# Kernel optimization log

Measured on AMD Instinct MI355X. Metric: run time of the kernel, lower is better.

## Reference

```python
import jax, jax.numpy as jnp
import numpy as np

N, E = 20000, 100000
D_IN, H1, C1 = 512, 8, 64   # conv1: 512 -> 8 heads x 64, concat -> 512
H2, C2 = 4, 128             # conv2: 512 -> 4 heads x 128, mean -> 128


def setup_inputs() -> dict:
    key = jax.random.key(0)
    k = jax.random.split(key, 12)
    s_in = 1.0 / np.sqrt(D_IN).astype(np.float32)
    return {
        "street_embedding": jax.random.normal(k[0], (N, D_IN), jnp.float32),
        "edge_index": jax.random.randint(k[1], (2, E), 0, N),
        "y": jax.random.randint(k[2], (N,), 0, C2),
        "train_mask": jax.random.bernoulli(k[3], 0.5, (N,)),
        "W1": jax.random.normal(k[4], (D_IN, H1 * C1), jnp.float32) * s_in,
        "att_src1": jax.random.normal(k[5], (H1, C1), jnp.float32) * 0.1,
        "att_dst1": jax.random.normal(k[6], (H1, C1), jnp.float32) * 0.1,
        "b1": jnp.zeros((H1 * C1,), jnp.float32),
        "W2": jax.random.normal(k[7], (H1 * C1, H2 * C2), jnp.float32) * s_in,
        "att_src2": jax.random.normal(k[8], (H2, C2), jnp.float32) * 0.1,
        "att_dst2": jax.random.normal(k[9], (H2, C2), jnp.float32) * 0.1,
        "b2": jnp.zeros((C2,), jnp.float32),
    }


def _gat_conv(x, W, a_src, a_dst, b, src, dst, n, H, C, concat):
    # linear transform (no bias, as in PyG GATConv's internal lin)
    xp = (x @ W).reshape(n, H, C)                      # [N,H,C]
    asrc = jnp.einsum('nhc,hc->nh', xp, a_src)         # [N,H]
    adst = jnp.einsum('nhc,hc->nh', xp, a_dst)
    e = jax.nn.leaky_relu(asrc[src] + adst[dst], 0.2)  # [E',H] edge scores
    # softmax over incoming edges per destination node
    m = jax.lax.stop_gradient(jax.ops.segment_max(e, dst, num_segments=n))
    ex = jnp.exp(e - m[dst])
    denom = jax.ops.segment_sum(ex, dst, num_segments=n)
    alpha = ex / (denom[dst] + 1e-16)                  # [E',H]
    out = jax.ops.segment_sum(alpha[:, :, None] * xp[src], dst, num_segments=n)  # [N,H,C]
    if concat:
        return out.reshape(n, H * C) + b
    return out.mean(axis=1) + b


def reference(street_embedding, edge_index, y, train_mask,
              W1, att_src1, att_dst1, b1, W2, att_src2, att_dst2, b2):
    n = street_embedding.shape[0]
    loop = jnp.arange(n)
    # PyG GATConv adds self-loops by default
    src = jnp.concatenate([edge_index[0], loop])
    dst = jnp.concatenate([edge_index[1], loop])
    # dropout layers are identity in eval mode
    h = _gat_conv(street_embedding, W1, att_src1, att_dst1, b1, src, dst, n, H1, C1, True)
    h = jax.nn.elu(h)
    out = _gat_conv(h, W2, att_src2, att_dst2, b2, src, dst, n, H2, C2, False)  # [N,C2]
    # CrossEntropyLoss, mean over train_mask nodes (weighted mean, jit-safe)
    logp = jax.nn.log_softmax(out, axis=-1)
    ce = -jnp.take_along_axis(logp, y[:, None], axis=-1)[:, 0]
    w = train_mask.astype(out.dtype)
    loss_su = jnp.sum(w * ce) / jnp.sum(w)
    return (loss_su, out)
```

## Files before the change

kernel.cpp:

```cpp
#include <hip/hip_runtime.h>
#include <cmath>

#define D_IN 512
#define HC   512
#define NH1  8
#define NC1  64
#define NH2  4
#define NC2  128
#define BM 128
#define BN 128
#define BK 64

typedef __attribute__((ext_vector_type(8))) short short8;
typedef __attribute__((ext_vector_type(4))) float f32x4;

__device__ inline ushort f2bf(float f) {
  unsigned u = __float_as_uint(f);
  return (ushort)((u + 0x7FFFu + ((u >> 16) & 1u)) >> 16);
}
__device__ inline float bf2f(ushort b) { return __uint_as_float(((unsigned)b) << 16); }

__global__ void k_cast_all(const float* __restrict__ x, ushort* __restrict__ Abf,
                           const float* __restrict__ W1, const float* __restrict__ W2,
                           ushort* __restrict__ Wt1, ushort* __restrict__ Wt2, int n4x) {
  const int KN = D_IN * HC;
  int i = blockIdx.x * blockDim.x + threadIdx.x;
  if (i < n4x) {
    float4 v = ((const float4*)x)[i];
    ushort4 r = { f2bf(v.x), f2bf(v.y), f2bf(v.z), f2bf(v.w) };
    ((ushort4*)Abf)[i] = r;
  } else {
    int idx = i - n4x;
    if (idx >= 2 * KN) return;
    const float* W = (idx < KN) ? W1 : W2;
    ushort* Wt = (idx < KN) ? Wt1 : Wt2;
    int j = (idx < KN) ? idx : idx - KN;
    int n = j / D_IN, k = j - n * D_IN;
    Wt[j] = f2bf(W[(size_t)k * HC + n]);
  }
}

template<int H>
__global__ void k_gemm_bf16(const ushort* __restrict__ A, const ushort* __restrict__ Bt,
                            ushort* __restrict__ Cbf,
                            const float* __restrict__ att_s, const float* __restrict__ att_d,
                            float* __restrict__ asrc, float* __restrict__ adst, int M) {
  constexpr int C = HC / H;
  __shared__ __align__(16) ushort As[BM * BK];
  __shared__ __align__(16) ushort Bs[BN * BK];
  int t = threadIdx.x;
  int m0 = blockIdx.y * BM;
  int n0 = blockIdx.x * BN;
  int wave = t >> 6, lane = t & 63;
  int ln = lane & 15, qd = lane >> 4;
  int wm = (wave >> 1) * 64, wn = (wave & 1) * 64;

  f32x4 acc[4][4] = {};

  int g = t >> 6, ct = (t >> 4) & 3, lt = t & 15;
  int rA0 = m0 + g * 16 + lt;      if (rA0 > M - 1) rA0 = M - 1;
  int rA1 = m0 + 64 + g * 16 + lt; if (rA1 > M - 1) rA1 = M - 1;
  const ushort* gA0 = A + (size_t)rA0 * D_IN + ct * 8;
  const ushort* gA1 = A + (size_t)rA1 * D_IN + ct * 8;
  const ushort* gB0 = Bt + (size_t)(n0 + g * 16 + lt) * D_IN + ct * 8;
  const ushort* gB1 = Bt + (size_t)(n0 + 64 + g * 16 + lt) * D_IN + ct * 8;

  for (int k0 = 0; k0 < D_IN; k0 += BK) {
    __syncthreads();
#pragma unroll
    for (int h = 0; h < 2; ++h) {
      int ko = k0 + h * 32;
      int lo = h * 4096;
      __builtin_amdgcn_global_load_lds(
          (const __attribute__((address_space(1))) void*)(gA0 + ko),
          (__attribute__((address_space(3))) void*)(As + lo + t * 8), 16, 0, 0);
      __builtin_amdgcn_global_load_lds(
          (const __attribute__((address_space(1))) void*)(gA1 + ko),
          (__attribute__((address_space(3))) void*)(As + lo + 2048 + t * 8), 16, 0, 0);
      __builtin_amdgcn_global_load_lds(
          (const __attribute__((address_space(1))) void*)(gB0 + ko),
          (__attribute__((address_space(3))) void*)(Bs + lo + t * 8), 16, 0, 0);
      __builtin_amdgcn_global_load_lds(
          (const __attribute__((address_space(1))) void*)(gB1 + ko),
          (__attribute__((address_space(3))) void*)(Bs + lo + 2048 + t * 8), 16, 0, 0);
    }
    __syncthreads();
#pragma unroll
    for (int h = 0; h < 2; ++h) {
      int lo = h * 4096;
      short8 a[4], bb[4];
#pragma unroll
      for (int i = 0; i < 4; ++i)
        a[i] = *(const short8*)&As[lo + (((wave >> 1) * 4 + i) * 4 + qd) * 128 + ln * 8];
#pragma unroll
      for (int j = 0; j < 4; ++j)
        bb[j] = *(const short8*)&Bs[lo + (((wave & 1) * 4 + j) * 4 + qd) * 128 + ln * 8];
#pragma unroll
      for (int i = 0; i < 4; ++i)
#pragma unroll
        for (int j = 0; j < 4; ++j)
          acc[i][j] = __builtin_amdgcn_mfma_f32_16x16x32_bf16(a[i], bb[j], acc[i][j], 0, 0, 0);
    }
  }

#pragma unroll
  for (int i = 0; i < 4; ++i) {
#pragma unroll
    for (int reg = 0; reg < 4; ++reg) {
      int row = m0 + wm + i * 16 + qd * 4 + reg;
      if (row >= M) continue;
#pragma unroll
      for (int j = 0; j < 4; ++j)
        Cbf[(size_t)row * HC + n0 + wn + j * 16 + ln] = f2bf(acc[i][j][reg]);
    }
  }

  int colbase = n0 + wn;
  int h = colbase / C;
  float sa[4], da[4];
#pragma unroll
  for (int j = 0; j < 4; ++j) {
    int c = (colbase % C) + j * 16 + ln;
    sa[j] = att_s[h * C + c];
    da[j] = att_d[h * C + c];
  }
#pragma unroll
  for (int i = 0; i < 4; ++i) {
#pragma unroll
    for (int reg = 0; reg < 4; ++reg) {
      float ps = acc[i][0][reg] * sa[0] + acc[i][1][reg] * sa[1]
               + acc[i][2][reg] * sa[2] + acc[i][3][reg] * sa[3];
      float pd = acc[i][0][reg] * da[0] + acc[i][1][reg] * da[1]
               + acc[i][2][reg] * da[2] + acc[i][3][reg] * da[3];
#pragma unroll
      for (int o = 1; o < 16; o <<= 1) { ps += __shfl_xor(ps, o); pd += __shfl_xor(pd, o); }
      int row = m0 + wm + i * 16 + qd * 4 + reg;
      if (ln == 0 && row < M) {
        if (C == 64) {
          asrc[row * H + h] = ps; adst[row * H + h] = pd;
        } else {
          int sub = (colbase >> 6) & 1;
          asrc[(row * H + h) * 2 + sub] = ps;
          adst[(row * H + h) * 2 + sub] = pd;
        }
      }
    }
  }
}

__global__ void k_hist(const int* __restrict__ ei, int E, int Etot, int* __restrict__ cnt) {
  int e = blockIdx.x * blockDim.x + threadIdx.x;
  if (e >= Etot) return;
  int d = (e < E) ? ei[E + e] : e - E;
  atomicAdd(&cnt[d], 1);
}

__global__ void k_scan(const int* __restrict__ cnt, int* __restrict__ rowstart, int N) {
  int tid = threadIdx.x;
  int T = (N + 1023) / 1024;
  int base = tid * T;
  int sum = 0;
  for (int i = 0; i < T; ++i) { int j = base + i; if (j < N) sum += cnt[j]; }
  int lane = tid & 63, w = tid >> 6;
  int v = sum;
#pragma unroll
  for (int off = 1; off < 64; off <<= 1) {
    int u = __shfl_up(v, off);
    if (lane >= off) v += u;
  }
  __shared__ int wsum[16];
  if (lane == 63) wsum[w] = v;
  __syncthreads();
  if (tid < 16) {
    int tv = wsum[tid];
#pragma unroll
    for (int off = 1; off < 16; off <<= 1) {
      int u = __shfl_up(tv, off);
      if (tid >= off) tv += u;
    }
    wsum[tid] = tv;
  }
  __syncthreads();
  int wave_prefix = (w == 0) ? 0 : wsum[w - 1];
  int run = wave_prefix + v - sum;
  for (int i = 0; i < T; ++i) {
    int j = base + i;
    if (j < N) { rowstart[j] = run; run += cnt[j]; }
  }
  if (tid == 1023) rowstart[N] = run;
}

__global__ void k_scatter(const int* __restrict__ ei, int E, int Etot,
                          const int* __restrict__ rowstart, int* __restrict__ cursor,
                          int* __restrict__ csr_src) {
  int e = blockIdx.x * blockDim.x + threadIdx.x;
  if (e >= Etot) return;
  int s = (e < E) ? ei[e] : e - E;
  int d = (e < E) ? ei[E + e] : e - E;
  int pos = atomicAdd(&cursor[d], 1);
  csr_src[rowstart[d] + pos] = s;
}

template<int H, int MODE>
__global__ void k_agg(const int* __restrict__ rowstart, const int* __restrict__ csr_src,
                      const float* __restrict__ asrc, const float* __restrict__ adst,
                      const ushort* __restrict__ xp, ushort* __restrict__ hout,
                      float* __restrict__ out2, const float* __restrict__ bias,
                      const int* __restrict__ y, const int* __restrict__ msk,
                      float* __restrict__ acc2, int N) {
  int n = blockIdx.x;
  int tid = threadIdx.x;
  constexpr int C = HC / H;
  int h = (tid * 4) / C;
  int beg = rowstart[n], end = rowstart[n + 1];

  __shared__ int   s_src[32];
  __shared__ float s_out[512];

  float adn = (MODE == 1) ? adst[n * H + h]
                          : adst[(n * H + h) * 2] + adst[(n * H + h) * 2 + 1];
  float ax = 0.f, ay = 0.f, az = 0.f, aw = 0.f, wsum = 0.f;

#define SCORE(s) ((MODE == 1) ? asrc[(s) * H + h] \
                              : asrc[((s) * H + h) * 2] + asrc[((s) * H + h) * 2 + 1])

  for (int c0 = beg; c0 < end; c0 += 32) {
    int len = end - c0; if (len > 32) len = 32;
    __syncthreads();
    if (tid < len) s_src[tid] = csr_src[c0 + tid];
    __syncthreads();
    int i = 0;
    for (; i + 1 < len; i += 2) {
      int s0 = s_src[i], s1 = s_src[i + 1];
      float v0 = SCORE(s0) + adn;
      float v1 = SCORE(s1) + adn;
      ushort4 a0 = ((const ushort4*)xp)[(size_t)s0 * 128 + tid];
      ushort4 a1 = ((const ushort4*)xp)[(size_t)s1 * 128 + tid];
      v0 = (v0 > 0.f) ? v0 : 0.2f * v0;
      v1 = (v1 > 0.f) ? v1 : 0.2f * v1;
      float w0 = __expf(v0), w1 = __expf(v1);
      ax += w0 * bf2f(a0.x) + w1 * bf2f(a1.x);
      ay += w0 * bf2f(a0.y) + w1 * bf2f(a1.y);
      az += w0 * bf2f(a0.z) + w1 * bf2f(a1.z);
      aw += w0 * bf2f(a0.w) + w1 * bf2f(a1.w);
      wsum += w0 + w1;
    }
    if (i < len) {
      int s0 = s_src[i];
      float v0 = SCORE(s0) + adn;
      ushort4 a0 = ((const ushort4*)xp)[(size_t)s0 * 128 + tid];
      v0 = (v0 > 0.f) ? v0 : 0.2f * v0;
      float w0 = __expf(v0);
      ax += w0 * bf2f(a0.x); ay += w0 * bf2f(a0.y);
      az += w0 * bf2f(a0.z); aw += w0 * bf2f(a0.w);
      wsum += w0;
    }
  }
#undef SCORE
  float rdn = 1.0f / (wsum + 1e-16f);
  ax *= rdn; ay *= rdn; az *= rdn; aw *= rdn;

  if (MODE == 1) {
    int hc = tid * 4;
    float v0 = ax + bias[hc], v1 = ay + bias[hc + 1];
    float v2 = az + bias[hc + 2], v3 = aw + bias[hc + 3];
    v0 = (v0 > 0.f) ? v0 : expm1f(v0);
    v1 = (v1 > 0.f) ? v1 : expm1f(v1);
    v2 = (v2 > 0.f) ? v2 : expm1f(v2);
    v3 = (v3 > 0.f) ? v3 : expm1f(v3);
    ushort4 rr = { f2bf(v0), f2bf(v1), f2bf(v2), f2bf(v3) };
    ((ushort4*)hout)[(size_t)n * 128 + tid] = rr;
  } else {
    int hc = tid * 4;
    s_out[hc] = ax; s_out[hc + 1] = ay; s_out[hc + 2] = az; s_out[hc + 3] = aw;
    __syncthreads();
    if (tid < 32) {
#pragma unroll
      for (int k = 0; k < 4; ++k) {
        int c = tid * 4 + k;
        float sum = s_out[c] + s_out[128 + c] + s_out[256 + c] + s_out[384 + c];
        float lg = sum * 0.25f + bias[c];
        out2[(size_t)n * NC2 + c] = lg;
        s_out[c] = lg;
      }
    }
    __syncthreads();
    float lv = s_out[tid];
    int lane = tid & 63, wv = tid >> 6;
    float mx = lv;
#pragma unroll
    for (int o = 32; o > 0; o >>= 1) mx = fmaxf(mx, __shfl_xor(mx, o));
    if (lane == 0) s_out[256 + wv] = mx;
    __syncthreads();
    mx = fmaxf(s_out[256], s_out[257]);
    float e = __expf(lv - mx);
#pragma unroll
    for (int o = 32; o > 0; o >>= 1) e += __shfl_xor(e, o);
    if (lane == 0) s_out[260 + wv] = e;
    __syncthreads();
    if (tid == 0 && msk[n] != 0) {
      float se = s_out[260] + s_out[261];
      float ce = mx + logf(se) - s_out[y[n]];
      int slot = n & 127;
      atomicAdd(&acc2[slot], ce);
      atomicAdd(&acc2[128 + slot], 1.0f);
    }
  }
}

__global__ void k_final(const float* __restrict__ acc2, float* __restrict__ out0) {
  int tid = threadIdx.x;
  float ce = acc2[tid], ct = acc2[128 + tid];
#pragma unroll
  for (int o = 32; o > 0; o >>= 1) { ce += __shfl_xor(ce, o); ct += __shfl_xor(ct, o); }
  __shared__ float s[4];
  if ((tid & 63) == 0) { s[(tid >> 6) * 2] = ce; s[(tid >> 6) * 2 + 1] = ct; }
  __syncthreads();
  if (tid == 0) out0[0] = (s[0] + s[2]) / (s[1] + s[3]);
}

extern "C" void kernel_launch(void* const* d_in, const int* in_sizes, int n_in,
                              void* d_out, int out_size, void* d_ws, size_t ws_size,
                              hipStream_t stream) {
  const float* x   = (const float*)d_in[0];
  const int*   ei  = (const int*)d_in[1];
  const int*   y   = (const int*)d_in[2];
  const int*   msk = (const int*)d_in[3];
  const float* W1  = (const float*)d_in[4];
  const float* as1 = (const float*)d_in[5];
  const float* ad1 = (const float*)d_in[6];
  const float* b1  = (const float*)d_in[7];
  const float* W2  = (const float*)d_in[8];
  const float* as2 = (const float*)d_in[9];
  const float* ad2 = (const float*)d_in[10];
  const float* b2  = (const float*)d_in[11];
  float* out = (float*)d_out;

  int N = in_sizes[0] / D_IN;
  int E = in_sizes[1] / 2;
  int Etot = E + N;

  float* ws = (float*)d_ws;
  size_t NF = (size_t)N * HC;
  float* asr1 = ws;
  float* adt1 = asr1 + (size_t)N * NH1;
  float* asr2 = adt1 + (size_t)N * NH1;
  float* adt2 = asr2 + (size_t)N * 2 * NH2;
  float* acc2 = adt2 + (size_t)N * 2 * NH2;
  int*   cnt    = (int*)(acc2 + 256);
  int*   cursor = cnt + N;
  size_t zero_bytes = (256 + 2 * (size_t)N) * sizeof(float);
  int*   rowstart = cursor + N;
  int*   csr_src  = rowstart + N + 1;
  ushort* xpbf = (ushort*)((((uintptr_t)(csr_src + Etot)) + 15) & ~(uintptr_t)15);
  ushort* Abf = xpbf + NF;
  ushort* Wt1 = Abf + NF;
  ushort* Wt2 = Wt1 + (size_t)D_IN * HC;

  hipMemsetAsync(acc2, 0, zero_bytes, stream);

  int n4x = (int)(NF / 4);
  int cast_total = n4x + 2 * D_IN * HC;
  k_cast_all<<<(cast_total + 255) / 256, 256, 0, stream>>>(x, Abf, W1, W2, Wt1, Wt2, n4x);

  k_hist<<<(Etot + 255) / 256, 256, 0, stream>>>(ei, E, Etot, cnt);
  k_scan<<<1, 1024, 0, stream>>>(cnt, rowstart, N);
  k_scatter<<<(Etot + 255) / 256, 256, 0, stream>>>(ei, E, Etot, rowstart, cursor, csr_src);

  dim3 ggrid(HC / BN, (N + BM - 1) / BM);

  k_gemm_bf16<NH1><<<ggrid, 256, 0, stream>>>(Abf, Wt1, xpbf, as1, ad1, asr1, adt1, N);
  k_agg<NH1, 1><<<N, 128, 0, stream>>>(rowstart, csr_src, asr1, adt1, xpbf, Abf,
                                       nullptr, b1, nullptr, nullptr, nullptr, N);

  k_gemm_bf16<NH2><<<ggrid, 256, 0, stream>>>(Abf, Wt2, xpbf, as2, ad2, asr2, adt2, N);
  k_agg<NH2, 2><<<N, 128, 0, stream>>>(rowstart, csr_src, asr2, adt2, xpbf, nullptr,
                                       out + 1, b2, y, msk, acc2, N);

  k_final<<<1, 128, 0, stream>>>(acc2, out);
}
```

Measured before the change: 287.8 us.

## Map one wavefront per destination node in GAT aggregation kernels

The aggregation kernels now assign one 64-lane wavefront per node, four nodes per 256-thread block, instead of a 128-thread block per node. Each lane loads 16-byte short8 rows, and edge indices come straight from global memory rather than through LDS with block barriers. The second layer's head mean and cross-entropy reduction use intra-wave shuffles instead of shared memory and __syncthreads. This removes block-level synchronisation and shrinks the grid, at the cost of more registers per lane and possible load imbalance between the four nodes sharing a block.

```diff
diff --git a/kernel.cpp b/kernel.cpp
--- a/kernel.cpp
+++ b/kernel.cpp
@@ -202,105 +202,99 @@
 }
 
 template<int H, int MODE>
-__global__ void k_agg(const int* __restrict__ rowstart, const int* __restrict__ csr_src,
-                      const float* __restrict__ asrc, const float* __restrict__ adst,
-                      const ushort* __restrict__ xp, ushort* __restrict__ hout,
-                      float* __restrict__ out2, const float* __restrict__ bias,
-                      const int* __restrict__ y, const int* __restrict__ msk,
-                      float* __restrict__ acc2, int N) {
-  int n = blockIdx.x;
-  int tid = threadIdx.x;
+__global__ __launch_bounds__(256)
+void k_agg(const int* __restrict__ rowstart, const int* __restrict__ csr_src,
+           const float* __restrict__ asrc, const float* __restrict__ adst,
+           const ushort* __restrict__ xp, ushort* __restrict__ hout,
+           float* __restrict__ out2, const float* __restrict__ bias,
+           const int* __restrict__ y, const int* __restrict__ msk,
+           float* __restrict__ acc2, int N) {
   constexpr int C = HC / H;
-  int h = (tid * 4) / C;
-  int beg = rowstart[n], end = rowstart[n + 1];
-
-  __shared__ int   s_src[32];
-  __shared__ float s_out[512];
+  int wave = threadIdx.x >> 6, lane = threadIdx.x & 63;
+  int n = blockIdx.x * 4 + wave;
+  if (n >= N) return;
+  int h = (lane * 8) / C;
 
   float adn = (MODE == 1) ? adst[n * H + h]
                           : adst[(n * H + h) * 2] + adst[(n * H + h) * 2 + 1];
-  float ax = 0.f, ay = 0.f, az = 0.f, aw = 0.f, wsum = 0.f;
+  float acc[8] = {};
+  float wsum = 0.f;
+  int beg = rowstart[n], end = rowstart[n + 1];
 
 #define SCORE(s) ((MODE == 1) ? asrc[(s) * H + h] \
                               : asrc[((s) * H + h) * 2] + asrc[((s) * H + h) * 2 + 1])
 
-  for (int c0 = beg; c0 < end; c0 += 32) {
-    int len = end - c0; if (len > 32) len = 32;
-    __syncthreads();
-    if (tid < len) s_src[tid] = csr_src[c0 + tid];
-    __syncthreads();
-    int i = 0;
-    for (; i + 1 < len; i += 2) {
-      int s0 = s_src[i], s1 = s_src[i + 1];
-      float v0 = SCORE(s0) + adn;
-      float v1 = SCORE(s1) + adn;
-      ushort4 a0 = ((const ushort4*)xp)[(size_t)s0 * 128 + tid];
-      ushort4 a1 = ((const ushort4*)xp)[(size_t)s1 * 128 + tid];
-      v0 = (v0 > 0.f) ? v0 : 0.2f * v0;
-      v1 = (v1 > 0.f) ? v1 : 0.2f * v1;
-      float w0 = __expf(v0), w1 = __expf(v1);
-      ax += w0 * bf2f(a0.x) + w1 * bf2f(a1.x);
-      ay += w0 * bf2f(a0.y) + w1 * bf2f(a1.y);
-      az += w0 * bf2f(a0.z) + w1 * bf2f(a1.z);
-      aw += w0 * bf2f(a0.w) + w1 * bf2f(a1.w);
-      wsum += w0 + w1;
-    }
-    if (i < len) {
-      int s0 = s_src[i];
-      float v0 = SCORE(s0) + adn;
-      ushort4 a0 = ((const ushort4*)xp)[(size_t)s0 * 128 + tid];
-      v0 = (v0 > 0.f) ? v0 : 0.2f * v0;
-      float w0 = __expf(v0);
-      ax += w0 * bf2f(a0.x); ay += w0 * bf2f(a0.y);
-      az += w0 * bf2f(a0.z); aw += w0 * bf2f(a0.w);
-      wsum += w0;
-    }
+  int i = beg;
+  for (; i + 1 < end; i += 2) {
+    int s0 = csr_src[i], s1 = csr_src[i + 1];
+    float v0 = SCORE(s0) + adn;
+    float v1 = SCORE(s1) + adn;
+    short8 r0 = ((const short8*)xp)[(size_t)s0 * 64 + lane];
+    short8 r1 = ((const short8*)xp)[(size_t)s1 * 64 + lane];
+    v0 = (v0 > 0.f) ? v0 : 0.2f * v0;
+    v1 = (v1 > 0.f) ? v1 : 0.2f * v1;
+    float w0 = __expf(v0), w1 = __expf(v1);
+#pragma unroll
+    for (int k = 0; k < 8; ++k)
+      acc[k] += w0 * bf2f((ushort)r0[k]) + w1 * bf2f((ushort)r1[k]);
+    wsum += w0 + w1;
+  }
+  if (i < end) {
+    int s0 = csr_src[i];
+    float v0 = SCORE(s0) + adn;
+    short8 r0 = ((const short8*)xp)[(size_t)s0 * 64 + lane];
+    v0 = (v0 > 0.f) ? v0 : 0.2f * v0;
+    float w0 = __expf(v0);
+#pragma unroll
+    for (int k = 0; k < 8; ++k) acc[k] += w0 * bf2f((ushort)r0[k]);
+    wsum += w0;
   }
 #undef SCORE
+
   float rdn = 1.0f / (wsum + 1e-16f);
-  ax *= rdn; ay *= rdn; az *= rdn; aw *= rdn;
+#pragma unroll
+  for (int k = 0; k < 8; ++k) acc[k] *= rdn;
 
   if (MODE == 1) {
-    int hc = tid * 4;
-    float v0 = ax + bias[hc], v1 = ay + bias[hc + 1];
-    float v2 = az + bias[hc + 2], v3 = aw + bias[hc + 3];
-    v0 = (v0 > 0.f) ? v0 : expm1f(v0);
-    v1 = (v1 > 0.f) ? v1 : expm1f(v1);
-    v2 = (v2 > 0.f) ? v2 : expm1f(v2);
-    v3 = (v3 > 0.f) ? v3 : expm1f(v3);
-    ushort4 rr = { f2bf(v0), f2bf(v1), f2bf(v2), f2bf(v3) };
-    ((ushort4*)hout)[(size_t)n * 128 + tid] = rr;
+    short8 rr;
+#pragma unroll
+    for (int k = 0; k < 8; ++k) {
+      float v = acc[k] + bias[lane * 8 + k];
+      v = (v > 0.f) ? v : expm1f(v);
+      rr[k] = (short)f2bf(v);
+    }
+    ((short8*)hout)[(size_t)n * 64 + lane] = rr;
   } else {
-    int hc = tid * 4;
-    s_out[hc] = ax; s_out[hc + 1] = ay; s_out[hc + 2] = az; s_out[hc + 3] = aw;
-    __syncthreads();
-    if (tid < 32) {
-#pragma unroll
-      for (int k = 0; k < 4; ++k) {
-        int c = tid * 4 + k;
-        float sum = s_out[c] + s_out[128 + c] + s_out[256 + c] + s_out[384 + c];
-        float lg = sum * 0.25f + bias[c];
-        out2[(size_t)n * NC2 + c] = lg;
-        s_out[c] = lg;
-      }
-    }
-    __syncthreads();
-    float lv = s_out[tid];
-    int lane = tid & 63, wv = tid >> 6;
-    float mx = lv;
-#pragma unroll
-    for (int o = 32; o > 0; o >>= 1) mx = fmaxf(mx, __shfl_xor(mx, o));
-    if (lane == 0) s_out[256 + wv] = mx;
-    __syncthreads();
-    mx = fmaxf(s_out[256], s_out[257]);
-    float e = __expf(lv - mx);
-#pragma unroll
-    for (int o = 32; o > 0; o >>= 1) e += __shfl_xor(e, o);
-    if (lane == 0) s_out[260 + wv] = e;
-    __syncthreads();
-    if (tid == 0 && msk[n] != 0) {
-      float se = s_out[260] + s_out[261];
-      float ce = mx + logf(se) - s_out[y[n]];
+    float lg[8];
+#pragma unroll
+    for (int k = 0; k < 8; ++k) {
+      float v = acc[k];
+      v += __shfl_xor(v, 16);
+      v += __shfl_xor(v, 32);
+      lg[k] = v * 0.25f + bias[(lane & 15) * 8 + k];
+    }
+    if (lane < 16) {
+#pragma unroll
+      for (int k = 0; k < 8; ++k)
+        out2[(size_t)n * NC2 + lane * 8 + k] = lg[k];
+    }
+    float mx = lg[0];
+#pragma unroll
+    for (int k = 1; k < 8; ++k) mx = fmaxf(mx, lg[k]);
+#pragma unroll
+    for (int o = 1; o < 16; o <<= 1) mx = fmaxf(mx, __shfl_xor(mx, o));
+    float se = 0.f;
+#pragma unroll
+    for (int k = 0; k < 8; ++k) se += __expf(lg[k] - mx);
+#pragma unroll
+    for (int o = 1; o < 16; o <<= 1) se += __shfl_xor(se, o);
+    int ty = y[n];
+    float myv = lg[0];
+#pragma unroll
+    for (int k = 1; k < 8; ++k) myv = ((ty & 7) == k) ? lg[k] : myv;
+    float tlg = __shfl(myv, ty >> 3);
+    if (lane == 0 && msk[n] != 0) {
+      float ce = mx + logf(se) - tlg;
       int slot = n & 127;
       atomicAdd(&acc2[slot], ce);
       atomicAdd(&acc2[128 + slot], 1.0f);
@@ -368,14 +362,15 @@
   k_scatter<<<(Etot + 255) / 256, 256, 0, stream>>>(ei, E, Etot, rowstart, cursor, csr_src);
 
   dim3 ggrid(HC / BN, (N + BM - 1) / BM);
+  int agrid = (N + 3) / 4;
 
   k_gemm_bf16<NH1><<<ggrid, 256, 0, stream>>>(Abf, Wt1, xpbf, as1, ad1, asr1, adt1, N);
-  k_agg<NH1, 1><<<N, 128, 0, stream>>>(rowstart, csr_src, asr1, adt1, xpbf, Abf,
-                                       nullptr, b1, nullptr, nullptr, nullptr, N);
+  k_agg<NH1, 1><<<agrid, 256, 0, stream>>>(rowstart, csr_src, asr1, adt1, xpbf, Abf,
+                                           nullptr, b1, nullptr, nullptr, nullptr, N);
 
   k_gemm_bf16<NH2><<<ggrid, 256, 0, stream>>>(Abf, Wt2, xpbf, as2, ad2, asr2, adt2, N);
-  k_agg<NH2, 2><<<N, 128, 0, stream>>>(rowstart, csr_src, asr2, adt2, xpbf, nullptr,
-                                       out + 1, b2, y, msk, acc2, N);
+  k_agg<NH2, 2><<<agrid, 256, 0, stream>>>(rowstart, csr_src, asr2, adt2, xpbf, nullptr,
+                                           out + 1, b2, y, msk, acc2, N);
 
   k_final<<<1, 128, 0, stream>>>(acc2, out);
 }
```

Measured after the change: 300.8 us. +4.5%, slower.
